# Kernel tuning notes

Measured on AMD Instinct MI355X. Metric: run time of the kernel, lower is better.

The kernel has to match this reference:

```python
import jax, jax.numpy as jnp
import numpy as np

N = 8192        # number of nodes (dense adjacency)
IN_DIM = 128    # GCN in_dim
OUT_DIM = 128   # GCN out_dim
MASK_THRESH = 0.8
NEG_INF = 1e9


def setup_inputs() -> dict:
    key = jax.random.key(0)
    kA, kX, kW = jax.random.split(key, 3)
    A = jax.random.uniform(kA, (N, N), dtype=jnp.float32)
    X = jax.random.normal(kX, (N, IN_DIM), dtype=jnp.float32)
    # nn.Linear(in_dim, out_dim): weight [out_dim, in_dim], bias [out_dim]
    W = jax.random.normal(kW, (OUT_DIM, IN_DIM), dtype=jnp.float32) * (1.0 / np.sqrt(IN_DIM))
    b = jnp.zeros((OUT_DIM,), dtype=jnp.float32)
    return {"A": A, "X": X, "W": W, "b": b}


def reference(A, X, W, b):
    # GCN.forward: A_norm = softmax(A - 1e9 * (A <= 0.8), axis=-1)
    # out = leaky_relu(A_norm @ Linear(X))   (relu=True path)
    logits = A - NEG_INF * (A <= MASK_THRESH).astype(A.dtype)   # [N, N]
    A_norm = jax.nn.softmax(logits, axis=-1)                     # row-wise softmax
    XW = X @ W.T + b                                             # [N, OUT_DIM]
    return jax.nn.leaky_relu(A_norm @ XW, negative_slope=0.01)   # [N, OUT_DIM]
```

## Files before the change

kernel.cpp:

```cpp
#include <hip/hip_runtime.h>
#include <hip/hip_bf16.h>

#define N_NODES 8192
#define DIM 128
#define MASK_THRESH 0.8f
#define RB 512
#define KSTEP 128

using f32x4  = __attribute__((ext_vector_type(4))) float;
using bf16x8 = __attribute__((ext_vector_type(8))) short;

static __device__ __forceinline__ short f2bf(float f) {
    unsigned u = __builtin_bit_cast(unsigned, f);
    u += 0x7fffu + ((u >> 16) & 1u);
    return (short)(u >> 16);
}

static __device__ __forceinline__ void gload16(const void* gsrc, void* ldst) {
    __builtin_amdgcn_global_load_lds(
        (const __attribute__((address_space(1))) unsigned int*)gsrc,
        (__attribute__((address_space(3))) unsigned int*)ldst,
        16, 0, 0);
}

__global__ __launch_bounds__(256) void build_vf_kernel(
    const float* __restrict__ X, const float* __restrict__ W,
    const float* __restrict__ bias, short* __restrict__ Vf) {
    __shared__ float xs[32][128];
    const int jt = blockIdx.x * 32;
    for (int e = threadIdx.x; e < 32 * 128; e += 256) {
        xs[e >> 7][e & 127] = X[(size_t)(jt + (e >> 7)) * DIM + (e & 127)];
    }
    __syncthreads();
    const int d  = threadIdx.x & 127;
    const int jh = threadIdx.x >> 7;
    float bv = bias[d];
    float acc[16];
#pragma unroll
    for (int i = 0; i < 16; i++) acc[i] = bv;
    const float* wrow = W + (size_t)d * DIM;
    for (int k = 0; k < DIM; k += 4) {
        f32x4 wv = *(const f32x4*)(wrow + k);
#pragma unroll
        for (int i = 0; i < 16; i++) {
            f32x4 xv = *(const f32x4*)(&xs[jh * 16 + i][k]);
            acc[i] = fmaf(xv[0], wv[0], acc[i]);
            acc[i] = fmaf(xv[1], wv[1], acc[i]);
            acc[i] = fmaf(xv[2], wv[2], acc[i]);
            acc[i] = fmaf(xv[3], wv[3], acc[i]);
        }
    }
    bf16x8 o0, o1;
#pragma unroll
    for (int i = 0; i < 8; i++) { o0[i] = f2bf(acc[i]); o1[i] = f2bf(acc[8 + i]); }
    const int kb = jt >> 5;
    const int t  = d >> 4;
    short* base = Vf + ((size_t)(kb * 8 + t) * 64 + (d & 15) + 32 * jh) * 8;
    *(bf16x8*)(base)       = o0;
    *(bf16x8*)(base + 128) = o1;
}

template <int WRITE_PARTIAL>
__global__ __launch_bounds__(256, 4) void fused_kernel(
    const float* __restrict__ A, const short* __restrict__ Vf,
    float* __restrict__ dst, float* __restrict__ Zp, int kchunk) {

    __shared__ __align__(16) float smem[8448];
    __shared__ float zs[4][16];

    const int tid   = threadIdx.x;
    const int w     = tid >> 6;
    const int lane  = tid & 63;
    const int row_a = lane & 15;
    const int kg    = lane >> 4;
    const int rb    = blockIdx.x & (RB - 1);
    const int chunk = blockIdx.x >> 9;
    const int r0    = rb * 16;
    const int k0    = chunk * kchunk;
    const int nsteps = kchunk >> 7;

    const float* asrc[2]; int adst_off[2];
#pragma unroll
    for (int i = 0; i < 2; i++) {
        const int arow = w * 4 + i * 2 + (lane >> 5);
        asrc[i] = A + (size_t)(r0 + arow) * N_NODES + k0 + (((lane & 31) ^ (arow & 7)) << 2);
        adst_off[i] = (w * 4 + i * 2) * 128;
    }
    const int aoff0 = row_a * 128 + (((w * 8 + kg * 2 + 0) ^ (row_a & 7)) << 2);
    const int aoff1 = row_a * 128 + (((w * 8 + kg * 2 + 1) ^ (row_a & 7)) << 2);
    const short* vfp = Vf + ((size_t)((k0 >> 5) + w) * 8 * 64 + lane) * 8;

    f32x4 acc[8];
#pragma unroll
    for (int t = 0; t < 8; t++) acc[t] = (f32x4)0.0f;
    float zacc = 0.0f;

#pragma unroll
    for (int i = 0; i < 2; i++) gload16(asrc[i], smem + adst_off[i]);

    for (int ks = 0; ks < nsteps; ks++) {
        __syncthreads();
        if (ks + 1 < nsteps) {
            float* nbuf = smem + ((ks + 1) & 1) * 2048;
#pragma unroll
            for (int i = 0; i < 2; i++)
                gload16(asrc[i] + (size_t)(ks + 1) * KSTEP, nbuf + adst_off[i]);
        }
        const float* ab = smem + (ks & 1) * 2048;
        const f32x4 av0 = *(const f32x4*)(ab + aoff0);
        const f32x4 av1 = *(const f32x4*)(ab + aoff1);
        float p[8];
#pragma unroll
        for (int i = 0; i < 4; i++) {
            p[i]     = (av0[i] > MASK_THRESH) ? __expf(av0[i]) : 0.0f;
            p[i + 4] = (av1[i] > MASK_THRESH) ? __expf(av1[i]) : 0.0f;
        }
        bf16x8 af;
#pragma unroll
        for (int i = 0; i < 8; i++) { zacc += p[i]; af[i] = f2bf(p[i]); }
        const short* vstep = vfp + (size_t)ks * 16384;
#pragma unroll
        for (int t = 0; t < 8; t++) {
            const bf16x8 bv = *(const bf16x8*)(vstep + t * 512);
            acc[t] = __builtin_amdgcn_mfma_f32_16x16x32_bf16(af, bv, acc[t], 0, 0, 0);
        }
    }

    zacc += __shfl_xor(zacc, 16);
    zacc += __shfl_xor(zacc, 32);
    if (lane < 16) zs[w][lane] = zacc;

    __syncthreads();
    float* accs = smem;
#pragma unroll
    for (int t = 0; t < 8; t++)
#pragma unroll
        for (int r = 0; r < 4; r++)
            accs[(w * 16 + kg * 4 + r) * 132 + t * 16 + row_a] = acc[t][r];
    __syncthreads();

    {
        const int row = tid >> 4;
        const int c8  = (tid & 15) * 8;
        float zt = zs[0][row] + zs[1][row] + zs[2][row] + zs[3][row];
        f32x4 s0 = (f32x4)0.0f, s1 = (f32x4)0.0f;
#pragma unroll
        for (int ww = 0; ww < 4; ww++) {
            const float* pp = &accs[(ww * 16 + row) * 132 + c8];
            s0 += *(const f32x4*)(pp);
            s1 += *(const f32x4*)(pp + 4);
        }
        if (WRITE_PARTIAL) {
            float* nd = dst + ((size_t)chunk * N_NODES + r0 + row) * DIM + c8;
            *(f32x4*)(nd)     = s0;
            *(f32x4*)(nd + 4) = s1;
            if (tid < 16) Zp[(size_t)chunk * N_NODES + r0 + tid] =
                zs[0][tid] + zs[1][tid] + zs[2][tid] + zs[3][tid];
        } else {
            f32x4 o0, o1;
#pragma unroll
            for (int j = 0; j < 4; j++) {
                float v0 = s0[j] / zt, v1 = s1[j] / zt;
                o0[j] = (v0 > 0.0f) ? v0 : 0.01f * v0;
                o1[j] = (v1 > 0.0f) ? v1 : 0.01f * v1;
            }
            float* od = dst + (size_t)(r0 + row) * DIM + c8;
            *(f32x4*)(od)     = o0;
            *(f32x4*)(od + 4) = o1;
        }
    }
}

__global__ __launch_bounds__(256) void reduce_kernel(
    const float* __restrict__ num, const float* __restrict__ Zp,
    float* __restrict__ out, int S) {
    const size_t i4 = (size_t)blockIdx.x * 256 + threadIdx.x;
    const int r  = (int)(i4 >> 5);
    const int c4 = (int)(i4 & 31) * 4;
    f32x4 s = (f32x4)0.0f;
    float z = 0.0f;
    for (int p = 0; p < S; p++) {
        s += *(const f32x4*)(num + ((size_t)p * N_NODES + r) * DIM + c4);
        z += Zp[(size_t)p * N_NODES + r];
    }
    f32x4 o;
#pragma unroll
    for (int j = 0; j < 4; j++) {
        const float v = s[j] / z;
        o[j] = (v > 0.0f) ? v : 0.01f * v;
    }
    *(f32x4*)(out + (size_t)r * DIM + c4) = o;
}

extern "C" void kernel_launch(void* const* d_in, const int* in_sizes, int n_in,
                              void* d_out, int out_size, void* d_ws, size_t ws_size,
                              hipStream_t stream) {
    const float* A = (const float*)d_in[0];
    const float* X = (const float*)d_in[1];
    const float* W = (const float*)d_in[2];
    const float* b = (const float*)d_in[3];
    float* out = (float*)d_out;

    const size_t VF_BYTES = (size_t)DIM * N_NODES * 2;
    short* Vf = (short*)d_ws;
    build_vf_kernel<<<N_NODES / 32, 256, 0, stream>>>(X, W, b, Vf);

    const size_t per_split = ((size_t)N_NODES * DIM + N_NODES) * sizeof(float);
    int S = 1;
    for (int cand = 4; cand >= 1; cand >>= 1) {
        if (VF_BYTES + (size_t)cand * per_split <= ws_size) { S = cand; break; }
    }

    if (S >= 2) {
        float* num = (float*)((char*)d_ws + VF_BYTES);
        float* Zp  = num + (size_t)S * N_NODES * DIM;
        fused_kernel<1><<<RB * S, 256, 0, stream>>>(A, Vf, num, Zp, N_NODES / S);
        reduce_kernel<<<(N_NODES * DIM / 4) / 256, 256, 0, stream>>>(num, Zp, out, S);
    } else {
        fused_kernel<0><<<RB, 256, 0, stream>>>(A, Vf, out, nullptr, N_NODES);
    }
}
```

Baseline: 125.1 us.

## Retile fused softmax-GEMM to 128-row blocks with 2x2 wave grid

Each block of the fused kernel now covers 128 rows (four waves in a 2x2 arrangement of 64 rows by 64 columns) instead of 16 rows, with a K step of 64 and a 64 KB double-buffered LDS tile for A. Each Vf fragment loaded from global memory is reused across four row groups, which cuts the repeated reads of Vf that the 16-row tiling forced. The block-level LDS reduction is removed and waves write their own output tiles directly, using scalar stores. Split-K can now go up to 8 chunks to keep the grid large, at the cost of more partial-sum traffic, lower occupancy (launch bounds 2) and higher register pressure.

```diff
diff --git a/kernel.cpp b/kernel.cpp
--- a/kernel.cpp
+++ b/kernel.cpp
@@ -4,8 +4,8 @@
 #define N_NODES 8192
 #define DIM 128
 #define MASK_THRESH 0.8f
-#define RB 512
-#define KSTEP 128
+#define RB 64
+#define KSTEP 64
 
 using f32x4  = __attribute__((ext_vector_type(4))) float;
 using bf16x8 = __attribute__((ext_vector_type(8))) short;
@@ -61,113 +61,126 @@
 }
 
 template <int WRITE_PARTIAL>
-__global__ __launch_bounds__(256, 4) void fused_kernel(
+__global__ __launch_bounds__(256, 2) void fused_kernel(
     const float* __restrict__ A, const short* __restrict__ Vf,
     float* __restrict__ dst, float* __restrict__ Zp, int kchunk) {
 
-    __shared__ __align__(16) float smem[8448];
-    __shared__ float zs[4][16];
+    __shared__ __align__(16) float abuf[16384];
+    __shared__ float zs[2][64];
 
     const int tid   = threadIdx.x;
-    const int w     = tid >> 6;
+    const int wid   = tid >> 6;
     const int lane  = tid & 63;
     const int row_a = lane & 15;
     const int kg    = lane >> 4;
+    const int wr    = wid & 1;
+    const int wc    = wid >> 1;
     const int rb    = blockIdx.x & (RB - 1);
-    const int chunk = blockIdx.x >> 9;
-    const int r0    = rb * 16;
+    const int chunk = blockIdx.x >> 6;
+    const int r0    = rb * 128;
     const int k0    = chunk * kchunk;
-    const int nsteps = kchunk >> 7;
-
-    const float* asrc[2]; int adst_off[2];
-#pragma unroll
-    for (int i = 0; i < 2; i++) {
-        const int arow = w * 4 + i * 2 + (lane >> 5);
-        asrc[i] = A + (size_t)(r0 + arow) * N_NODES + k0 + (((lane & 31) ^ (arow & 7)) << 2);
-        adst_off[i] = (w * 4 + i * 2) * 128;
-    }
-    const int aoff0 = row_a * 128 + (((w * 8 + kg * 2 + 0) ^ (row_a & 7)) << 2);
-    const int aoff1 = row_a * 128 + (((w * 8 + kg * 2 + 1) ^ (row_a & 7)) << 2);
-    const short* vfp = Vf + ((size_t)((k0 >> 5) + w) * 8 * 64 + lane) * 8;
-
-    f32x4 acc[8];
-#pragma unroll
-    for (int t = 0; t < 8; t++) acc[t] = (f32x4)0.0f;
-    float zacc = 0.0f;
-
-#pragma unroll
-    for (int i = 0; i < 2; i++) gload16(asrc[i], smem + adst_off[i]);
+    const int nsteps = kchunk >> 6;
+
+    f32x4 acc[4][4];
+#pragma unroll
+    for (int rg = 0; rg < 4; rg++)
+#pragma unroll
+        for (int t = 0; t < 4; t++) acc[rg][t] = (f32x4)0.0f;
+    float zacc[4] = {0.0f, 0.0f, 0.0f, 0.0f};
+
+    const int sub   = lane >> 4;
+    const int schnk = lane & 15;
+
+#pragma unroll
+    for (int i = 0; i < 8; i++) {
+        const int row_s = wid * 32 + i * 4 + sub;
+        gload16(A + (size_t)(r0 + row_s) * N_NODES + k0 + ((schnk ^ (row_s & 15)) << 2),
+                abuf + (wid * 32 + i * 4) * 64);
+    }
 
     for (int ks = 0; ks < nsteps; ks++) {
         __syncthreads();
         if (ks + 1 < nsteps) {
-            float* nbuf = smem + ((ks + 1) & 1) * 2048;
-#pragma unroll
-            for (int i = 0; i < 2; i++)
-                gload16(asrc[i] + (size_t)(ks + 1) * KSTEP, nbuf + adst_off[i]);
-        }
-        const float* ab = smem + (ks & 1) * 2048;
-        const f32x4 av0 = *(const f32x4*)(ab + aoff0);
-        const f32x4 av1 = *(const f32x4*)(ab + aoff1);
-        float p[8];
-#pragma unroll
-        for (int i = 0; i < 4; i++) {
-            p[i]     = (av0[i] > MASK_THRESH) ? __expf(av0[i]) : 0.0f;
-            p[i + 4] = (av1[i] > MASK_THRESH) ? __expf(av1[i]) : 0.0f;
-        }
-        bf16x8 af;
-#pragma unroll
-        for (int i = 0; i < 8; i++) { zacc += p[i]; af[i] = f2bf(p[i]); }
-        const short* vstep = vfp + (size_t)ks * 16384;
-#pragma unroll
-        for (int t = 0; t < 8; t++) {
-            const bf16x8 bv = *(const bf16x8*)(vstep + t * 512);
-            acc[t] = __builtin_amdgcn_mfma_f32_16x16x32_bf16(af, bv, acc[t], 0, 0, 0);
-        }
-    }
-
-    zacc += __shfl_xor(zacc, 16);
-    zacc += __shfl_xor(zacc, 32);
-    if (lane < 16) zs[w][lane] = zacc;
-
+            float* nb = abuf + ((ks + 1) & 1) * 8192;
+#pragma unroll
+            for (int i = 0; i < 8; i++) {
+                const int row_s = wid * 32 + i * 4 + sub;
+                gload16(A + (size_t)(r0 + row_s) * N_NODES + k0 + (ks + 1) * KSTEP
+                          + ((schnk ^ (row_s & 15)) << 2),
+                        nb + (wid * 32 + i * 4) * 64);
+            }
+        }
+        const float* ab = abuf + (ks & 1) * 8192;
+        const int kb_glob = (k0 >> 5) + ks * 2;
+#pragma unroll
+        for (int kb = 0; kb < 2; kb++) {
+            bf16x8 bv[4];
+#pragma unroll
+            for (int t = 0; t < 4; t++)
+                bv[t] = *(const bf16x8*)(Vf + ((size_t)(kb_glob + kb) * 8 + wc * 4 + t) * 512 + lane * 8);
+#pragma unroll
+            for (int rg = 0; rg < 4; rg++) {
+                const int row  = wr * 64 + rg * 16 + row_a;
+                const int base = row * 64;
+                const int c0   = kb * 8 + kg * 2;
+                const f32x4 av0 = *(const f32x4*)(ab + base + (((c0 + 0) ^ row_a) << 2));
+                const f32x4 av1 = *(const f32x4*)(ab + base + (((c0 + 1) ^ row_a) << 2));
+                float p[8];
+#pragma unroll
+                for (int i = 0; i < 4; i++) {
+                    p[i]     = (av0[i] > MASK_THRESH) ? __expf(av0[i]) : 0.0f;
+                    p[i + 4] = (av1[i] > MASK_THRESH) ? __expf(av1[i]) : 0.0f;
+                }
+                bf16x8 af;
+#pragma unroll
+                for (int i = 0; i < 8; i++) { zacc[rg] += p[i]; af[i] = f2bf(p[i]); }
+#pragma unroll
+                for (int t = 0; t < 4; t++)
+                    acc[rg][t] = __builtin_amdgcn_mfma_f32_16x16x32_bf16(af, bv[t], acc[rg][t], 0, 0, 0);
+            }
+        }
+    }
+
+#pragma unroll
+    for (int rg = 0; rg < 4; rg++) {
+        zacc[rg] += __shfl_xor(zacc[rg], 16);
+        zacc[rg] += __shfl_xor(zacc[rg], 32);
+    }
+    if (wc == 0 && lane < 16) {
+#pragma unroll
+        for (int rg = 0; rg < 4; rg++) zs[wr][rg * 16 + lane] = zacc[rg];
+    }
     __syncthreads();
-    float* accs = smem;
-#pragma unroll
-    for (int t = 0; t < 8; t++)
-#pragma unroll
-        for (int r = 0; r < 4; r++)
-            accs[(w * 16 + kg * 4 + r) * 132 + t * 16 + row_a] = acc[t][r];
-    __syncthreads();
-
-    {
-        const int row = tid >> 4;
-        const int c8  = (tid & 15) * 8;
-        float zt = zs[0][row] + zs[1][row] + zs[2][row] + zs[3][row];
-        f32x4 s0 = (f32x4)0.0f, s1 = (f32x4)0.0f;
-#pragma unroll
-        for (int ww = 0; ww < 4; ww++) {
-            const float* pp = &accs[(ww * 16 + row) * 132 + c8];
-            s0 += *(const f32x4*)(pp);
-            s1 += *(const f32x4*)(pp + 4);
-        }
-        if (WRITE_PARTIAL) {
-            float* nd = dst + ((size_t)chunk * N_NODES + r0 + row) * DIM + c8;
-            *(f32x4*)(nd)     = s0;
-            *(f32x4*)(nd + 4) = s1;
-            if (tid < 16) Zp[(size_t)chunk * N_NODES + r0 + tid] =
-                zs[0][tid] + zs[1][tid] + zs[2][tid] + zs[3][tid];
-        } else {
-            f32x4 o0, o1;
-#pragma unroll
-            for (int j = 0; j < 4; j++) {
-                float v0 = s0[j] / zt, v1 = s1[j] / zt;
-                o0[j] = (v0 > 0.0f) ? v0 : 0.01f * v0;
-                o1[j] = (v1 > 0.0f) ? v1 : 0.01f * v1;
-            }
-            float* od = dst + (size_t)(r0 + row) * DIM + c8;
-            *(f32x4*)(od)     = o0;
-            *(f32x4*)(od + 4) = o1;
-        }
+
+    if (WRITE_PARTIAL) {
+        float* nd = dst + (size_t)chunk * N_NODES * DIM;
+#pragma unroll
+        for (int rg = 0; rg < 4; rg++)
+#pragma unroll
+            for (int t = 0; t < 4; t++)
+#pragma unroll
+                for (int r = 0; r < 4; r++) {
+                    const int row = r0 + wr * 64 + rg * 16 + kg * 4 + r;
+                    const int col = wc * 64 + t * 16 + row_a;
+                    nd[(size_t)row * DIM + col] = acc[rg][t][r];
+                }
+        if (wc == 0 && lane < 16) {
+#pragma unroll
+            for (int rg = 0; rg < 4; rg++)
+                Zp[(size_t)chunk * N_NODES + r0 + wr * 64 + rg * 16 + lane] = zacc[rg];
+        }
+    } else {
+#pragma unroll
+        for (int rg = 0; rg < 4; rg++)
+#pragma unroll
+            for (int t = 0; t < 4; t++)
+#pragma unroll
+                for (int r = 0; r < 4; r++) {
+                    const int row = r0 + wr * 64 + rg * 16 + kg * 4 + r;
+                    const int col = wc * 64 + t * 16 + row_a;
+                    const float v = acc[rg][t][r] / zs[wr][rg * 16 + kg * 4 + r];
+                    dst[(size_t)row * DIM + col] = (v > 0.0f) ? v : 0.01f * v;
+                }
     }
 }
 
@@ -207,7 +220,7 @@
 
     const size_t per_split = ((size_t)N_NODES * DIM + N_NODES) * sizeof(float);
     int S = 1;
-    for (int cand = 4; cand >= 1; cand >>= 1) {
+    for (int cand = 8; cand >= 1; cand >>= 1) {
         if (VF_BYTES + (size_t)cand * per_split <= ws_size) { S = cand; break; }
     }
 
```

Result: no change. 125.8 us (+0.6%).
